# Performance work log

Hardware: AMD Instinct MI355X
Metric: run time of the kernel (lower is better)

Reference implementation:

```python
import jax, jax.numpy as jnp
import numpy as np

B, NQ, NK = 4, 2048, 2048
D_MODEL, D_K, D_V, H = 1024, 1024, 1024, 16


def setup_inputs() -> dict:
    key = jax.random.key(0)
    ks = jax.random.split(key, 8)
    return {
        "queries": jax.random.normal(ks[0], (B, NQ, D_MODEL), dtype=jnp.float32),
        "keys": jax.random.normal(ks[1], (B, NK, D_MODEL), dtype=jnp.float32),
        "values": jax.random.normal(ks[2], (B, NK, D_MODEL), dtype=jnp.float32),
        # nn.Linear weights init.normal_(std=0.001); stored here in (in, out) layout
        "Wq": jax.random.normal(ks[3], (D_MODEL, D_K), dtype=jnp.float32) * 0.001,
        "Wk": jax.random.normal(ks[4], (D_MODEL, D_K), dtype=jnp.float32) * 0.001,
        "Wv": jax.random.normal(ks[5], (D_MODEL, D_V), dtype=jnp.float32) * 0.001,
        "Wo": jax.random.normal(ks[6], (D_V, D_MODEL), dtype=jnp.float32) * 0.001,
        "bo": jnp.zeros((D_MODEL,), dtype=jnp.float32),
    }


def reference(queries, keys, values, Wq, Wk, Wv, Wo, bo):
    b_s, nq, _ = queries.shape
    nk = keys.shape[1]
    hd_k = D_K // H  # per-head key dim
    hd_v = D_V // H  # per-head value dim
    # projections -> [b, h, n, hd]
    q = (queries @ Wq).reshape(b_s, nq, H, hd_k).transpose(0, 2, 1, 3)
    k = (keys @ Wk).reshape(b_s, nk, H, hd_k).transpose(0, 2, 1, 3)
    v = (values @ Wv).reshape(b_s, nk, H, hd_v).transpose(0, 2, 1, 3)
    # NOTE: original scales by sqrt(d_k) (full d_k), not per-head dim
    att = jnp.einsum("bhqd,bhkd->bhqk", q, k) / np.float32(np.sqrt(D_K))
    att = jax.nn.softmax(att, axis=-1)
    # dropout = identity (eval mode)
    out = jnp.einsum("bhqk,bhkd->bhqd", att, v)
    out = out.transpose(0, 2, 1, 3).reshape(b_s, nq, D_V)
    return out @ Wo + bo
```

## Files before the change

### kernel.cpp

```cpp
#include <hip/hip_runtime.h>


#define DM    1024
#define NSEQ  2048
#define HEADS 16
#define HD    64

typedef float floatx4 __attribute__((ext_vector_type(4)));
typedef short s16x4   __attribute__((ext_vector_type(4)));
typedef short s16x8   __attribute__((ext_vector_type(8)));
typedef unsigned int u32x4 __attribute__((ext_vector_type(4)));

static __device__ __forceinline__ floatx4 mfma_bf16(s16x8 a, s16x8 b, floatx4 c) {
  return __builtin_amdgcn_mfma_f32_16x16x32_bf16(a, b, c, 0, 0, 0);
}

static __device__ __forceinline__ void gload_lds16(const void* g, void* l) {
  __builtin_amdgcn_global_load_lds(
      (const __attribute__((address_space(1))) unsigned*)g,
      (__attribute__((address_space(3))) unsigned*)l, 16, 0, 0);
}

static __device__ __forceinline__ short f2bf(float f) {
  unsigned u = __builtin_bit_cast(unsigned, f);
  u += 0x7FFFu + ((u >> 16) & 1u);
  return (short)(u >> 16);
}

static __device__ __forceinline__ unsigned cvtpk_bf16(float lo, float hi) {
  unsigned r;
  asm("v_cvt_pk_bf16_f32 %0, %1, %2" : "=v"(r) : "v"(lo), "v"(hi));
  return r;
}

static __device__ __forceinline__ unsigned pack2_bf16(float a, float b) {
  unsigned ua = __builtin_bit_cast(unsigned, a) + 0x8000u;
  unsigned ub = __builtin_bit_cast(unsigned, b) + 0x8000u;
#if __has_builtin(__builtin_amdgcn_perm)
  return __builtin_amdgcn_perm(ub, ua, 0x07060302u);
#else
  return (ub & 0xffff0000u) | (ua >> 16);
#endif
}

__global__ __launch_bounds__(256) void transpose_cast_w(
    const float* __restrict__ W0, const float* __restrict__ W1,
    const float* __restrict__ W2, const float* __restrict__ W3,
    short* __restrict__ T0, short* __restrict__ T1,
    short* __restrict__ T2, short* __restrict__ T3) {
  __shared__ float tile[32][33];
  const float* W = blockIdx.z == 0 ? W0 : blockIdx.z == 1 ? W1 : blockIdx.z == 2 ? W2 : W3;
  short*       T = blockIdx.z == 0 ? T0 : blockIdx.z == 1 ? T1 : blockIdx.z == 2 ? T2 : T3;
  const int bx = blockIdx.x * 32;
  const int by = blockIdx.y * 32;
  const int tx = threadIdx.x, ty = threadIdx.y;
  for (int i = 0; i < 4; i++)
    tile[ty + i * 8][tx] = W[(long)(by + ty + i * 8) * DM + bx + tx];
  __syncthreads();
  for (int i = 0; i < 4; i++)
    T[(long)(bx + ty + i * 8) * DM + by + tx] = f2bf(tile[tx][ty + i * 8]);
}

__global__ __launch_bounds__(256, 2) void proj_kernel(
    const float* __restrict__ Aq, const float* __restrict__ Ak, const float* __restrict__ Av,
    const short* __restrict__ BtQ, const short* __restrict__ BtK, const short* __restrict__ BtV,
    short* __restrict__ Qh, short* __restrict__ Kh, short* __restrict__ Vt) {
  __shared__ short lds[2 * 8192];
  const int z = blockIdx.z;
  const float* A  = z == 0 ? Aq  : z == 1 ? Ak  : Av;
  const short* Bt = z == 0 ? BtQ : z == 1 ? BtK : BtV;
  const int t = threadIdx.x;
  const int w = t >> 6, l = t & 63, quad = l >> 4, lm = l & 15;
  const int wm = w >> 1, wn = w & 1;
  const int row0 = blockIdx.x * 128, col0 = blockIdx.y * 128;

  floatx4 acc[4][4];
  for (int mi = 0; mi < 4; mi++)
    for (int ni = 0; ni < 4; ni++) acc[mi][ni] = (floatx4){0.f, 0.f, 0.f, 0.f};

  floatx4 ar[4];
  auto loadA = [&](int k0) __attribute__((always_inline)) {
    {
      int c = t, g = c >> 6, q = (c >> 4) & 3, rm = c & 15;
      const float* p = A + (long)(row0 + g * 16 + rm) * DM + k0 + q * 8;
      ar[0] = *(const floatx4*)p;
      ar[1] = *(const floatx4*)(p + 4);
    }
    {
      int c = t + 256, g = c >> 6, q = (c >> 4) & 3, rm = c & 15;
      const float* p = A + (long)(row0 + g * 16 + rm) * DM + k0 + q * 8;
      ar[2] = *(const floatx4*)p;
      ar[3] = *(const floatx4*)(p + 4);
    }
  };
  auto writeA = [&](int buf) __attribute__((always_inline)) {
    short* base = lds + buf * 8192;
    u32x4 w0 = {cvtpk_bf16(ar[0][0], ar[0][1]), cvtpk_bf16(ar[0][2], ar[0][3]),
                cvtpk_bf16(ar[1][0], ar[1][1]), cvtpk_bf16(ar[1][2], ar[1][3])};
    u32x4 w1 = {cvtpk_bf16(ar[2][0], ar[2][1]), cvtpk_bf16(ar[2][2], ar[2][3]),
                cvtpk_bf16(ar[3][0], ar[3][1]), cvtpk_bf16(ar[3][2], ar[3][3])};
    *(s16x8*)(base + t * 8)         = __builtin_bit_cast(s16x8, w0);
    *(s16x8*)(base + (t + 256) * 8) = __builtin_bit_cast(s16x8, w1);
  };
  auto stageB = [&](int k0, int buf) __attribute__((always_inline)) {
    short* base = lds + buf * 8192 + 4096;
#pragma unroll
    for (int i = 0; i < 2; i++) {
      int g = w * 2 + i;
      const short* src = Bt + (long)(col0 + g * 16 + lm) * DM + k0 + quad * 8;
      gload_lds16(src, base + g * 512);
    }
  };
  auto process = [&](int buf) __attribute__((always_inline)) {
    const short* base = lds + buf * 8192;
    s16x8 af[4], bfr[4];
#pragma unroll
    for (int mi = 0; mi < 4; mi++)
      af[mi] = *(const s16x8*)(base + (wm * 4 + mi) * 512 + l * 8);
#pragma unroll
    for (int ni = 0; ni < 4; ni++)
      bfr[ni] = *(const s16x8*)(base + 4096 + (wn * 4 + ni) * 512 + l * 8);
    __builtin_amdgcn_s_setprio(1);
#pragma unroll
    for (int mi = 0; mi < 4; mi++)
#pragma unroll
      for (int ni = 0; ni < 4; ni++)
        acc[mi][ni] = mfma_bf16(af[mi], bfr[ni], acc[mi][ni]);
    __builtin_amdgcn_s_setprio(0);
  };

  loadA(0);
  stageB(0, 0);
  writeA(0);
  __syncthreads();
  int cur = 0;
  for (int k0 = 0; k0 < DM; k0 += 32) {
    const int kn = (k0 + 32 < DM) ? k0 + 32 : 0;
    loadA(kn);
    stageB(kn, cur ^ 1);
    process(cur);
    writeA(cur ^ 1);
    __syncthreads();
    cur ^= 1;
  }

  const int rowbase = row0 + wm * 64;
  const int colbase = col0 + wn * 64;
  const int b = rowbase >> 11;
  const int h = colbase >> 6;
  const int rloc = rowbase & 2047;
  if (z < 2) {
    short* Out = z == 0 ? Qh : Kh;
    const float osc = z == 0 ? 0.0450842200277801f : 1.0f;
    long base = ((long)(b * HEADS + h)) * NSEQ * HD;
    for (int mi = 0; mi < 4; mi++)
      for (int r = 0; r < 4; r++) {
        int q = rloc + mi * 16 + quad * 4 + r;
        long rowoff = base + (long)q * HD + lm;
        for (int ni = 0; ni < 4; ni++)
          Out[rowoff + ni * 16] = f2bf(acc[mi][ni][r] * osc);
      }
  } else {
    long base = ((long)(b * HEADS + h)) * HD * NSEQ;
    for (int mi = 0; mi < 4; mi++)
      for (int r = 0; r < 4; r++) {
        int kcol = rloc + (mi >> 1) * 32 + quad * 8 + (mi & 1) * 4 + r;
        for (int ni = 0; ni < 4; ni++)
          Vt[base + (long)(ni * 16 + lm) * NSEQ + kcol] = f2bf(acc[mi][ni][r]);
      }
  }
}

__global__ __launch_bounds__(256, 2) void attn_kernel(
    const short* __restrict__ Qh, const short* __restrict__ Kh,
    const short* __restrict__ Vt, short* __restrict__ Obf) {
  __shared__ short lds[2 * 8192];
  const int t = threadIdx.x;
  const int w = t >> 6, l = t & 63, quad = l >> 4, lm = l & 15;
  const int bh = blockIdx.x;
  const int qtile = blockIdx.y * 128 + w * 32;
  const short* Qp = Qh + (long)bh * NSEQ * HD;
  const short* Kp = Kh + (long)bh * NSEQ * HD;
  const short* Vp = Vt + (long)bh * HD * NSEQ;

  s16x8 aq[2][2];
#pragma unroll
  for (int qi = 0; qi < 2; qi++)
#pragma unroll
    for (int c = 0; c < 2; c++)
      aq[qi][c] = *(const s16x8*)(Qp + (long)(qtile + qi * 16 + lm) * HD + c * 32 + quad * 8);

  floatx4 acc[2][4];
  float lsum[2] = {0.f, 0.f};
#pragma unroll
  for (int qi = 0; qi < 2; qi++)
#pragma unroll
    for (int n = 0; n < 4; n++) acc[qi][n] = (floatx4){0.f, 0.f, 0.f, 0.f};

  auto stage = [&](int kt, int buf) __attribute__((always_inline)) {
    short* base = lds + buf * 8192;
#pragma unroll
    for (int i = 0; i < 4; i++) {
      int g = w * 4 + i;
      const short* src;
      if (w < 2) {
        int s = (g >> 2) & 1, j = (g >> 1) & 1, c = g & 1;
        src = Kp + (long)(kt + s * 32 + j * 16 + lm) * HD + c * 32 + quad * 8;
      } else {
        int gg = g & 7;
        int s = gg >> 2, n = gg & 3;
        src = Vp + (long)(n * 16 + lm) * NSEQ + kt + s * 32 + quad * 8;
      }
      gload_lds16(src, base + g * 512);
    }
  };

  auto process = [&](const short* Lb, int s) __attribute__((always_inline)) {
    s16x8 bk[2][2];
#pragma unroll
    for (int j = 0; j < 2; j++)
#pragma unroll
      for (int c = 0; c < 2; c++)
        bk[j][c] = *(const s16x8*)(Lb + ((s * 4 + j * 2 + c) * 64 + l) * 8);
    s16x8 vraw[4];
#pragma unroll
    for (int n = 0; n < 4; n++)
      vraw[n] = *(const s16x8*)(Lb + ((8 + s * 4 + n) * 64 + l) * 8);
#pragma unroll
    for (int qi = 0; qi < 2; qi++) {
      floatx4 sT[2];
      sT[0] = (floatx4){0.f, 0.f, 0.f, 0.f};
      sT[1] = (floatx4){0.f, 0.f, 0.f, 0.f};
      __builtin_amdgcn_s_setprio(1);
#pragma unroll
      for (int c = 0; c < 2; c++) {
        sT[0] = mfma_bf16(bk[0][c], aq[qi][c], sT[0]);
        sT[1] = mfma_bf16(bk[1][c], aq[qi][c], sT[1]);
      }
      __builtin_amdgcn_s_setprio(0);
      float p0 = __builtin_amdgcn_exp2f(sT[0][0]);
      float p1 = __builtin_amdgcn_exp2f(sT[0][1]);
      float p2 = __builtin_amdgcn_exp2f(sT[0][2]);
      float p3 = __builtin_amdgcn_exp2f(sT[0][3]);
      float p4 = __builtin_amdgcn_exp2f(sT[1][0]);
      float p5 = __builtin_amdgcn_exp2f(sT[1][1]);
      float p6 = __builtin_amdgcn_exp2f(sT[1][2]);
      float p7 = __builtin_amdgcn_exp2f(sT[1][3]);
      lsum[qi] += ((p0 + p1) + (p2 + p3)) + ((p4 + p5) + (p6 + p7));
      u32x4 pw = {pack2_bf16(p0, p1), pack2_bf16(p2, p3),
                  pack2_bf16(p4, p5), pack2_bf16(p6, p7)};
      s16x8 pcat = __builtin_bit_cast(s16x8, pw);
      __builtin_amdgcn_s_setprio(1);
#pragma unroll
      for (int n = 0; n < 4; n++)
        acc[qi][n] = mfma_bf16(vraw[n], pcat, acc[qi][n]);
      __builtin_amdgcn_s_setprio(0);
    }
  };

  stage(0, 0);
  __syncthreads();
  int cur = 0;
  for (int kt = 0; kt < NSEQ; kt += 64) {
    if (kt + 64 < NSEQ) stage(kt + 64, cur ^ 1);
    const short* Lb = lds + cur * 8192;
    process(Lb, 0);
    process(Lb, 1);
    __syncthreads();
    cur ^= 1;
  }

  const int b = bh >> 4, h = bh & 15;
  short* Ow = lds + w * 1152;
  const int erow = l >> 2, ecg = l & 3;
#pragma unroll
  for (int qi = 0; qi < 2; qi++) {
    float ls = lsum[qi];
    ls += __shfl_xor(ls, 16);
    ls += __shfl_xor(ls, 32);
    float rl = 1.0f / ls;
#pragma unroll
    for (int n = 0; n < 4; n++)
#pragma unroll
      for (int r = 0; r < 4; r++)
        Ow[lm * 72 + n * 16 + quad * 4 + r] = f2bf(acc[qi][n][r] * rl);
    s16x8 o0 = *(const s16x8*)(Ow + erow * 72 + ecg * 16);
    s16x8 o1 = *(const s16x8*)(Ow + erow * 72 + ecg * 16 + 8);
    long gaddr = ((long)(b * NSEQ + qtile + qi * 16 + erow)) * DM + h * HD + ecg * 16;
    *(s16x8*)(Obf + gaddr) = o0;
    *(s16x8*)(Obf + gaddr + 8) = o1;
  }
}

__global__ __launch_bounds__(256, 2) void out_kernel(
    const short* __restrict__ Ab, const short* __restrict__ Bt,
    const float* __restrict__ bias, float* __restrict__ Out) {
  __shared__ short lds[2 * 8192];
  const int t = threadIdx.x;
  const int w = t >> 6, l = t & 63, quad = l >> 4, lm = l & 15;
  const int wm = w >> 1, wn = w & 1;
  const int row0 = blockIdx.x * 128, col0 = blockIdx.y * 128;

  floatx4 acc[4][4];
  for (int mi = 0; mi < 4; mi++)
    for (int ni = 0; ni < 4; ni++) acc[mi][ni] = (floatx4){0.f, 0.f, 0.f, 0.f};

  auto stage = [&](int k0, int buf) __attribute__((always_inline)) {
    short* base = lds + buf * 8192;
#pragma unroll
    for (int i = 0; i < 4; i++) {
      int g = w * 4 + i;
      const short* src = (g < 8)
          ? Ab + (long)(row0 + g * 16 + lm) * DM + k0 + quad * 8
          : Bt + (long)(col0 + (g - 8) * 16 + lm) * DM + k0 + quad * 8;
      gload_lds16(src, base + g * 512);
    }
  };
  auto process = [&](int buf) __attribute__((always_inline)) {
    const short* base = lds + buf * 8192;
    s16x8 af[4], bfr[4];
#pragma unroll
    for (int mi = 0; mi < 4; mi++)
      af[mi] = *(const s16x8*)(base + (wm * 4 + mi) * 512 + l * 8);
#pragma unroll
    for (int ni = 0; ni < 4; ni++)
      bfr[ni] = *(const s16x8*)(base + (8 + wn * 4 + ni) * 512 + l * 8);
    __builtin_amdgcn_s_setprio(1);
#pragma unroll
    for (int mi = 0; mi < 4; mi++)
#pragma unroll
      for (int ni = 0; ni < 4; ni++)
        acc[mi][ni] = mfma_bf16(af[mi], bfr[ni], acc[mi][ni]);
    __builtin_amdgcn_s_setprio(0);
  };

  stage(0, 0);
  __syncthreads();
  int cur = 0;
  for (int k0 = 0; k0 < DM; k0 += 32) {
    const int kn = (k0 + 32 < DM) ? k0 + 32 : 0;
    stage(kn, cur ^ 1);
    process(cur);
    __syncthreads();
    cur ^= 1;
  }

  const int rowbase = row0 + wm * 64;
  const int colbase = col0 + wn * 64;
  for (int mi = 0; mi < 4; mi++)
    for (int r = 0; r < 4; r++) {
      int gr = rowbase + mi * 16 + quad * 4 + r;
      for (int ni = 0; ni < 4; ni++) {
        int gc = colbase + ni * 16 + lm;
        Out[(long)gr * DM + gc] = acc[mi][ni][r] + bias[gc];
      }
    }
}

extern "C" void kernel_launch(void* const* d_in, const int* in_sizes, int n_in,
                              void* d_out, int out_size, void* d_ws, size_t ws_size,
                              hipStream_t stream) {
  (void)in_sizes; (void)n_in; (void)out_size; (void)ws_size;
  const float* queries = (const float*)d_in[0];
  const float* keys    = (const float*)d_in[1];
  const float* values  = (const float*)d_in[2];
  const float* Wq = (const float*)d_in[3];
  const float* Wk = (const float*)d_in[4];
  const float* Wv = (const float*)d_in[5];
  const float* Wo = (const float*)d_in[6];
  const float* bo = (const float*)d_in[7];
  float* out = (float*)d_out;

  char* ws = (char*)d_ws;
  const size_t MB = 1024 * 1024;
  short* WqT = (short*)(ws + 0 * MB);
  short* WkT = (short*)(ws + 2 * MB);
  short* WvT = (short*)(ws + 4 * MB);
  short* WoT = (short*)(ws + 6 * MB);
  short* Qh  = (short*)(ws + 8 * MB);
  short* Kh  = (short*)(ws + 24 * MB);
  short* Vt  = (short*)(ws + 40 * MB);
  short* Obf = (short*)(ws + 56 * MB);

  transpose_cast_w<<<dim3(32, 32, 4), dim3(32, 8), 0, stream>>>(
      Wq, Wk, Wv, Wo, WqT, WkT, WvT, WoT);
  proj_kernel<<<dim3(64, 8, 3), 256, 0, stream>>>(
      queries, keys, values, WqT, WkT, WvT, Qh, Kh, Vt);
  attn_kernel<<<dim3(64, 16), 256, 0, stream>>>(Qh, Kh, Vt, Obf);
  out_kernel<<<dim3(64, 8), 256, 0, stream>>>(Obf, WoT, bo, out);
}
```

Before: 389.6 us.

## Triple-buffer GEMM LDS pipelines and stream fp32 A directly into LDS

Both projection and output GEMMs move from double-buffered staging with a full __syncthreads per k-step to a three-stage ring. The ring uses explicit vmcnt waits and one barrier per iteration, so two tiles stay in flight. In the projection kernel the fp32 activations are now copied straight to LDS via global_load_lds instead of through registers, and converted to bf16 after reading back from LDS. This raises LDS use per block (72KB in proj), which may limit occupancy, and doubles LDS read bytes for A.

```diff
diff --git a/kernel.cpp b/kernel.cpp
--- a/kernel.cpp
+++ b/kernel.cpp
@@ -42,6 +42,8 @@
   return (ub & 0xffff0000u) | (ua >> 16);
 #endif
 }
+
+#define WAIT_VMCNT(N) asm volatile("s_waitcnt vmcnt(" #N ")" ::: "memory")
 
 __global__ __launch_bounds__(256) void transpose_cast_w(
     const float* __restrict__ W0, const float* __restrict__ W1,
@@ -65,7 +67,7 @@
     const float* __restrict__ Aq, const float* __restrict__ Ak, const float* __restrict__ Av,
     const short* __restrict__ BtQ, const short* __restrict__ BtK, const short* __restrict__ BtV,
     short* __restrict__ Qh, short* __restrict__ Kh, short* __restrict__ Vt) {
-  __shared__ short lds[2 * 8192];
+  __shared__ short lds[3 * 12288];
   const int z = blockIdx.z;
   const float* A  = z == 0 ? Aq  : z == 1 ? Ak  : Av;
   const short* Bt = z == 0 ? BtQ : z == 1 ? BtK : BtV;
@@ -78,48 +80,42 @@
   for (int mi = 0; mi < 4; mi++)
     for (int ni = 0; ni < 4; ni++) acc[mi][ni] = (floatx4){0.f, 0.f, 0.f, 0.f};
 
-  floatx4 ar[4];
-  auto loadA = [&](int k0) __attribute__((always_inline)) {
-    {
-      int c = t, g = c >> 6, q = (c >> 4) & 3, rm = c & 15;
-      const float* p = A + (long)(row0 + g * 16 + rm) * DM + k0 + q * 8;
-      ar[0] = *(const floatx4*)p;
-      ar[1] = *(const floatx4*)(p + 4);
-    }
-    {
-      int c = t + 256, g = c >> 6, q = (c >> 4) & 3, rm = c & 15;
-      const float* p = A + (long)(row0 + g * 16 + rm) * DM + k0 + q * 8;
-      ar[2] = *(const floatx4*)p;
-      ar[3] = *(const floatx4*)(p + 4);
-    }
-  };
-  auto writeA = [&](int buf) __attribute__((always_inline)) {
-    short* base = lds + buf * 8192;
-    u32x4 w0 = {cvtpk_bf16(ar[0][0], ar[0][1]), cvtpk_bf16(ar[0][2], ar[0][3]),
-                cvtpk_bf16(ar[1][0], ar[1][1]), cvtpk_bf16(ar[1][2], ar[1][3])};
-    u32x4 w1 = {cvtpk_bf16(ar[2][0], ar[2][1]), cvtpk_bf16(ar[2][2], ar[2][3]),
-                cvtpk_bf16(ar[3][0], ar[3][1]), cvtpk_bf16(ar[3][2], ar[3][3])};
-    *(s16x8*)(base + t * 8)         = __builtin_bit_cast(s16x8, w0);
-    *(s16x8*)(base + (t + 256) * 8) = __builtin_bit_cast(s16x8, w1);
-  };
-  auto stageB = [&](int k0, int buf) __attribute__((always_inline)) {
-    short* base = lds + buf * 8192 + 4096;
+  auto stage = [&](int k0, int buf) __attribute__((always_inline)) {
+    short* base = lds + buf * 12288;
+#pragma unroll
+    for (int i = 0; i < 4; i++) {
+      int g = w * 4 + i;
+      const float* src =
+          A + (long)(row0 + ((g >> 1) << 4) + lm) * DM + k0 + quad * 8 + (g & 1) * 4;
+      gload_lds16(src, base + g * 512);
+    }
 #pragma unroll
     for (int i = 0; i < 2; i++) {
-      int g = w * 2 + i;
-      const short* src = Bt + (long)(col0 + g * 16 + lm) * DM + k0 + quad * 8;
-      gload_lds16(src, base + g * 512);
-    }
-  };
+      int gb = w * 2 + i;
+      const short* src = Bt + (long)(col0 + gb * 16 + lm) * DM + k0 + quad * 8;
+      gload_lds16(src, base + 8192 + gb * 512);
+    }
+  };
+
   auto process = [&](int buf) __attribute__((always_inline)) {
-    const short* base = lds + buf * 8192;
-    s16x8 af[4], bfr[4];
-#pragma unroll
-    for (int mi = 0; mi < 4; mi++)
-      af[mi] = *(const s16x8*)(base + (wm * 4 + mi) * 512 + l * 8);
+    const short* base = lds + buf * 12288;
+    floatx4 alo[4], ahi[4];
+#pragma unroll
+    for (int mi = 0; mi < 4; mi++) {
+      alo[mi] = *(const floatx4*)(base + ((wm * 4 + mi) * 2 + 0) * 512 + l * 8);
+      ahi[mi] = *(const floatx4*)(base + ((wm * 4 + mi) * 2 + 1) * 512 + l * 8);
+    }
+    s16x8 bfr[4];
 #pragma unroll
     for (int ni = 0; ni < 4; ni++)
-      bfr[ni] = *(const s16x8*)(base + 4096 + (wn * 4 + ni) * 512 + l * 8);
+      bfr[ni] = *(const s16x8*)(base + 8192 + (wn * 4 + ni) * 512 + l * 8);
+    s16x8 af[4];
+#pragma unroll
+    for (int mi = 0; mi < 4; mi++) {
+      u32x4 p = {cvtpk_bf16(alo[mi][0], alo[mi][1]), cvtpk_bf16(alo[mi][2], alo[mi][3]),
+                 cvtpk_bf16(ahi[mi][0], ahi[mi][1]), cvtpk_bf16(ahi[mi][2], ahi[mi][3])};
+      af[mi] = __builtin_bit_cast(s16x8, p);
+    }
     __builtin_amdgcn_s_setprio(1);
 #pragma unroll
     for (int mi = 0; mi < 4; mi++)
@@ -129,20 +125,27 @@
     __builtin_amdgcn_s_setprio(0);
   };
 
-  loadA(0);
-  stageB(0, 0);
-  writeA(0);
-  __syncthreads();
+  stage(0, 0);
+  stage(32, 1);
   int cur = 0;
-  for (int k0 = 0; k0 < DM; k0 += 32) {
-    const int kn = (k0 + 32 < DM) ? k0 + 32 : 0;
-    loadA(kn);
-    stageB(kn, cur ^ 1);
+  for (int tt = 0; tt < 30; ++tt) {
+    WAIT_VMCNT(6);
+    __builtin_amdgcn_s_barrier();
+    __builtin_amdgcn_sched_barrier(0);
+    int nb = cur + 2 >= 3 ? cur - 1 : cur + 2;
+    stage((tt + 2) * 32, nb);
     process(cur);
-    writeA(cur ^ 1);
-    __syncthreads();
-    cur ^= 1;
+    cur = cur + 1 >= 3 ? 0 : cur + 1;
   }
+  WAIT_VMCNT(6);
+  __builtin_amdgcn_s_barrier();
+  __builtin_amdgcn_sched_barrier(0);
+  process(cur);
+  cur = cur + 1 >= 3 ? 0 : cur + 1;
+  WAIT_VMCNT(0);
+  __builtin_amdgcn_s_barrier();
+  __builtin_amdgcn_sched_barrier(0);
+  process(cur);
 
   const int rowbase = row0 + wm * 64;
   const int colbase = col0 + wn * 64;
@@ -295,7 +298,7 @@
 __global__ __launch_bounds__(256, 2) void out_kernel(
     const short* __restrict__ Ab, const short* __restrict__ Bt,
     const float* __restrict__ bias, float* __restrict__ Out) {
-  __shared__ short lds[2 * 8192];
+  __shared__ short lds[3 * 8192];
   const int t = threadIdx.x;
   const int w = t >> 6, l = t & 63, quad = l >> 4, lm = l & 15;
   const int wm = w >> 1, wn = w & 1;
@@ -335,15 +338,26 @@
   };
 
   stage(0, 0);
-  __syncthreads();
+  stage(32, 1);
   int cur = 0;
-  for (int k0 = 0; k0 < DM; k0 += 32) {
-    const int kn = (k0 + 32 < DM) ? k0 + 32 : 0;
-    stage(kn, cur ^ 1);
+  for (int tt = 0; tt < 30; ++tt) {
+    WAIT_VMCNT(4);
+    __builtin_amdgcn_s_barrier();
+    __builtin_amdgcn_sched_barrier(0);
+    int nb = cur + 2 >= 3 ? cur - 1 : cur + 2;
+    stage((tt + 2) * 32, nb);
     process(cur);
-    __syncthreads();
-    cur ^= 1;
+    cur = cur + 1 >= 3 ? 0 : cur + 1;
   }
+  WAIT_VMCNT(4);
+  __builtin_amdgcn_s_barrier();
+  __builtin_amdgcn_sched_barrier(0);
+  process(cur);
+  cur = cur + 1 >= 3 ? 0 : cur + 1;
+  WAIT_VMCNT(0);
+  __builtin_amdgcn_s_barrier();
+  __builtin_amdgcn_sched_barrier(0);
+  process(cur);
 
   const int rowbase = row0 + wm * 64;
   const int colbase = col0 + wn * 64;
```

Result: no change. 385.7 us (-1.0%).

## Widen projection tiles to 128x256 and triple-buffer output GEMM pipeline

Applied to the files above, without the earlier changes.

The projection kernel now uses 512 threads per block with a 128x256 output tile, so each block reuses its converted A tile across twice as many columns and halves the redundant fp32 A loads and conversions. The output GEMM moves from a double buffer with full __syncthreads to a three-stage LDS ring that waits on vmcnt counters, uses raw barriers and inline-asm ds_read_b128, so global-to-LDS loads stay two tiles ahead of the MFMAs. The cost is more LDS per block, which can lower occupancy, and hand-written waitcnt logic that depends on exact load counts.

```diff
diff --git a/kernel.cpp b/kernel.cpp
--- a/kernel.cpp
+++ b/kernel.cpp
@@ -20,6 +20,20 @@
       (const __attribute__((address_space(1))) unsigned*)g,
       (__attribute__((address_space(3))) unsigned*)l, 16, 0, 0);
 }
+
+static __device__ __forceinline__ unsigned lds_addr(const void* p) {
+  return (unsigned)(unsigned long long)p;
+}
+
+static __device__ __forceinline__ s16x8 ds_read_b128a(unsigned byteaddr) {
+  s16x8 r;
+  asm volatile("ds_read_b128 %0, %1" : "=v"(r) : "v"(byteaddr));
+  return r;
+}
+
+#define WAIT_LGKM0() \
+  { asm volatile("s_waitcnt lgkmcnt(0)" ::: "memory"); __builtin_amdgcn_sched_barrier(0); }
+#define WAIT_VMCNT(N) asm volatile("s_waitcnt vmcnt(" #N ")" ::: "memory")
 
 static __device__ __forceinline__ short f2bf(float f) {
   unsigned u = __builtin_bit_cast(unsigned, f);
@@ -61,49 +75,36 @@
     T[(long)(bx + ty + i * 8) * DM + by + tx] = f2bf(tile[tx][ty + i * 8]);
 }
 
-__global__ __launch_bounds__(256, 2) void proj_kernel(
+__global__ __launch_bounds__(512, 4) void proj_kernel(
     const float* __restrict__ Aq, const float* __restrict__ Ak, const float* __restrict__ Av,
     const short* __restrict__ BtQ, const short* __restrict__ BtK, const short* __restrict__ BtV,
     short* __restrict__ Qh, short* __restrict__ Kh, short* __restrict__ Vt) {
-  __shared__ short lds[2 * 8192];
+  __shared__ short lds[2 * 12288];
   const int z = blockIdx.z;
   const float* A  = z == 0 ? Aq  : z == 1 ? Ak  : Av;
   const short* Bt = z == 0 ? BtQ : z == 1 ? BtK : BtV;
   const int t = threadIdx.x;
   const int w = t >> 6, l = t & 63, quad = l >> 4, lm = l & 15;
-  const int wm = w >> 1, wn = w & 1;
-  const int row0 = blockIdx.x * 128, col0 = blockIdx.y * 128;
+  const int wm = w >> 2, wn = w & 3;
+  const int row0 = blockIdx.x * 128, col0 = blockIdx.y * 256;
 
   floatx4 acc[4][4];
   for (int mi = 0; mi < 4; mi++)
     for (int ni = 0; ni < 4; ni++) acc[mi][ni] = (floatx4){0.f, 0.f, 0.f, 0.f};
 
-  floatx4 ar[4];
+  floatx4 a0, a1;
   auto loadA = [&](int k0) __attribute__((always_inline)) {
-    {
-      int c = t, g = c >> 6, q = (c >> 4) & 3, rm = c & 15;
-      const float* p = A + (long)(row0 + g * 16 + rm) * DM + k0 + q * 8;
-      ar[0] = *(const floatx4*)p;
-      ar[1] = *(const floatx4*)(p + 4);
-    }
-    {
-      int c = t + 256, g = c >> 6, q = (c >> 4) & 3, rm = c & 15;
-      const float* p = A + (long)(row0 + g * 16 + rm) * DM + k0 + q * 8;
-      ar[2] = *(const floatx4*)p;
-      ar[3] = *(const floatx4*)(p + 4);
-    }
+    const float* p = A + (long)(row0 + w * 16 + lm) * DM + k0 + quad * 8;
+    a0 = *(const floatx4*)p;
+    a1 = *(const floatx4*)(p + 4);
   };
   auto writeA = [&](int buf) __attribute__((always_inline)) {
-    short* base = lds + buf * 8192;
-    u32x4 w0 = {cvtpk_bf16(ar[0][0], ar[0][1]), cvtpk_bf16(ar[0][2], ar[0][3]),
-                cvtpk_bf16(ar[1][0], ar[1][1]), cvtpk_bf16(ar[1][2], ar[1][3])};
-    u32x4 w1 = {cvtpk_bf16(ar[2][0], ar[2][1]), cvtpk_bf16(ar[2][2], ar[2][3]),
-                cvtpk_bf16(ar[3][0], ar[3][1]), cvtpk_bf16(ar[3][2], ar[3][3])};
-    *(s16x8*)(base + t * 8)         = __builtin_bit_cast(s16x8, w0);
-    *(s16x8*)(base + (t + 256) * 8) = __builtin_bit_cast(s16x8, w1);
+    u32x4 pk = {cvtpk_bf16(a0[0], a0[1]), cvtpk_bf16(a0[2], a0[3]),
+                cvtpk_bf16(a1[0], a1[1]), cvtpk_bf16(a1[2], a1[3])};
+    *(s16x8*)(lds + buf * 12288 + w * 512 + l * 8) = __builtin_bit_cast(s16x8, pk);
   };
   auto stageB = [&](int k0, int buf) __attribute__((always_inline)) {
-    short* base = lds + buf * 8192 + 4096;
+    short* base = lds + buf * 12288 + 4096;
 #pragma unroll
     for (int i = 0; i < 2; i++) {
       int g = w * 2 + i;
@@ -112,7 +113,7 @@
     }
   };
   auto process = [&](int buf) __attribute__((always_inline)) {
-    const short* base = lds + buf * 8192;
+    const short* base = lds + buf * 12288;
     s16x8 af[4], bfr[4];
 #pragma unroll
     for (int mi = 0; mi < 4; mi++)
@@ -295,7 +296,7 @@
 __global__ __launch_bounds__(256, 2) void out_kernel(
     const short* __restrict__ Ab, const short* __restrict__ Bt,
     const float* __restrict__ bias, float* __restrict__ Out) {
-  __shared__ short lds[2 * 8192];
+  __shared__ short lds[3 * 8192];
   const int t = threadIdx.x;
   const int w = t >> 6, l = t & 63, quad = l >> 4, lm = l & 15;
   const int wm = w >> 1, wn = w & 1;
@@ -316,15 +317,19 @@
       gload_lds16(src, base + g * 512);
     }
   };
+  const unsigned lds0 = lds_addr(lds);
   auto process = [&](int buf) __attribute__((always_inline)) {
-    const short* base = lds + buf * 8192;
+    const unsigned lbase = lds0 + buf * 16384;
+    const unsigned abase = lbase + wm * 4096 + l * 16;
+    const unsigned bbase = lbase + 8192 + wn * 4096 + l * 16;
     s16x8 af[4], bfr[4];
 #pragma unroll
     for (int mi = 0; mi < 4; mi++)
-      af[mi] = *(const s16x8*)(base + (wm * 4 + mi) * 512 + l * 8);
+      af[mi] = ds_read_b128a(abase + mi * 1024);
 #pragma unroll
     for (int ni = 0; ni < 4; ni++)
-      bfr[ni] = *(const s16x8*)(base + (8 + wn * 4 + ni) * 512 + l * 8);
+      bfr[ni] = ds_read_b128a(bbase + ni * 1024);
+    WAIT_LGKM0();
     __builtin_amdgcn_s_setprio(1);
 #pragma unroll
     for (int mi = 0; mi < 4; mi++)
@@ -335,15 +340,27 @@
   };
 
   stage(0, 0);
-  __syncthreads();
+  stage(32, 1);
   int cur = 0;
-  for (int k0 = 0; k0 < DM; k0 += 32) {
-    const int kn = (k0 + 32 < DM) ? k0 + 32 : 0;
-    stage(kn, cur ^ 1);
+  for (int tt = 0; tt < 30; ++tt) {
+    WAIT_VMCNT(4);
+    __builtin_amdgcn_s_barrier();
+    __builtin_amdgcn_sched_barrier(0);
+    int nb = cur + 2 >= 3 ? cur - 1 : cur + 2;
+    stage((tt + 2) * 32, nb);
+    __builtin_amdgcn_sched_barrier(0);
     process(cur);
-    __syncthreads();
-    cur ^= 1;
+    cur = cur + 1 >= 3 ? 0 : cur + 1;
   }
+  WAIT_VMCNT(4);
+  __builtin_amdgcn_s_barrier();
+  __builtin_amdgcn_sched_barrier(0);
+  process(cur);
+  cur = cur + 1 >= 3 ? 0 : cur + 1;
+  WAIT_VMCNT(0);
+  __builtin_amdgcn_s_barrier();
+  __builtin_amdgcn_sched_barrier(0);
+  process(cur);
 
   const int rowbase = row0 + wm * 64;
   const int colbase = col0 + wn * 64;
@@ -384,7 +401,7 @@
 
   transpose_cast_w<<<dim3(32, 32, 4), dim3(32, 8), 0, stream>>>(
       Wq, Wk, Wv, Wo, WqT, WkT, WvT, WoT);
-  proj_kernel<<<dim3(64, 8, 3), 256, 0, stream>>>(
+  proj_kernel<<<dim3(64, 4, 3), 512, 0, stream>>>(
       queries, keys, values, WqT, WkT, WvT, Qh, Kh, Vt);
   attn_kernel<<<dim3(64, 16), 256, 0, stream>>>(Qh, Kh, Vt, Obf);
   out_kernel<<<dim3(64, 8), 256, 0, stream>>>(Obf, WoT, bo, out);
```

Result: faster. 370.0 us (-5.0%).
